# Optimization experiments

Measured on AMD Instinct MI355X. Metric: run time of the kernel, lower is better.

Reference implementation:

```python
import jax, jax.numpy as jnp
import numpy as np

N_HEAD = 16
HEAD_DIM = 64  # n_embd // n_head = 1024 // 16

def setup_inputs() -> dict:
    key = jax.random.key(0)
    k1, k2, k3 = jax.random.split(key, 3)
    B, T, C = 4, 2048, 1024
    x = jax.random.normal(k1, (B, T, C), dtype=jnp.float32)
    w_qkv = jax.random.normal(k2, (3 * C, C), dtype=jnp.float32) * (C ** -0.5)
    w_proj = jax.random.normal(k3, (C, C), dtype=jnp.float32) * (C ** -0.5)
    b_proj = jnp.zeros((C,), dtype=jnp.float32)
    return {"x": x, "w_qkv": w_qkv, "w_proj": w_proj, "b_proj": b_proj}

def reference(x, w_qkv, w_proj, b_proj):
    B, T, C = x.shape
    H, hd = N_HEAD, HEAD_DIM
    # fused QKV projection (no bias), torch Linear: x @ W^T
    qkv = jnp.einsum('btc,dc->btd', x, w_qkv)           # [B,T,3C]
    # module-specific reshape: per-head groups of 3*hd, then chunk into q,k,v
    qkv = qkv.reshape(B, T, H, 3 * hd)
    q, k, v = jnp.split(qkv, 3, axis=-1)                # each [B,T,H,hd]
    q = q.transpose(0, 2, 1, 3)                         # [B,H,T,hd]
    k = k.transpose(0, 2, 1, 3)
    v = v.transpose(0, 2, 1, 3)
    att = jnp.einsum('bhqd,bhkd->bhqk', q, k) * (hd ** -0.5)
    causal = jnp.tril(jnp.ones((T, T), dtype=bool))
    att = jnp.where(causal, att, -jnp.inf)
    att = jax.nn.softmax(att, axis=-1)
    out = jnp.einsum('bhqk,bhkd->bhqd', att, v)         # [B,H,T,hd]
    out = out.transpose(0, 2, 1, 3).reshape(B, T, C)
    out = jnp.einsum('btc,dc->btd', out, w_proj) + b_proj
    return out
```

## Files before the change

kernel.cpp:

```cpp
#include <hip/hip_runtime.h>
#include <hip/hip_bf16.h>

typedef __attribute__((ext_vector_type(8))) short bf16x8;
typedef __attribute__((ext_vector_type(4))) float f32x4;
typedef __attribute__((ext_vector_type(16))) float f32x16;
typedef __attribute__((ext_vector_type(4))) int i32x4;
typedef unsigned short u16;

__device__ __forceinline__ u16 f2bf(float f) {
    __hip_bfloat16 h = __float2bfloat16(f);
    return __builtin_bit_cast(u16, h);
}
__device__ __forceinline__ bf16x8 load8(const u16* p) {
    return *reinterpret_cast<const bf16x8*>(p);
}
__device__ __forceinline__ void gl2lds16(const u16* g, u16* l) {
    __builtin_amdgcn_global_load_lds(
        (const __attribute__((address_space(1))) void*)g,
        (__attribute__((address_space(3))) void*)l, 16, 0, 0);
}
__device__ __forceinline__ unsigned int cvtpk(float lo, float hi) {
    unsigned int r;
    asm("v_cvt_pk_bf16_f32 %0, %1, %2" : "=v"(r) : "v"(lo), "v"(hi));
    return r;
}

#define QSCALE 0.1803368801111244f

__global__ __launch_bounds__(256) void cast_all(
    const float* __restrict__ x, const float* __restrict__ wq,
    const float* __restrict__ wp, u16* __restrict__ Xb,
    u16* __restrict__ Wqb, u16* __restrict__ Wpb)
{
    int i = blockIdx.x * blockDim.x + threadIdx.x;
    const float* s; u16* d; int j;
    if (i < 2097152)      { s = x;  d = Xb;  j = i; }
    else if (i < 2883584) { s = wq; d = Wqb; j = i - 2097152; }
    else                  { s = wp; d = Wpb; j = i - 2883584; }
    float4 f = reinterpret_cast<const float4*>(s)[j];
    ushort4 o;
    o.x = f2bf(f.x); o.y = f2bf(f.y); o.z = f2bf(f.z); o.w = f2bf(f.w);
    reinterpret_cast<ushort4*>(d)[j] = o;
}

#define GEMM256_BODY(EPILOGUE)                                                 \
    const int t = threadIdx.x;                                                 \
    const int lane = t & 63;                                                   \
    const int wave = t >> 6;                                                   \
    const int quad = (lane >> 4);                                              \
    const int lid  = lane & 15;                                                \
    const int wm = wave >> 1;                                                  \
    const int wn = wave & 1;                                                   \
    const int mtile = blockIdx.x * 256;                                        \
    const int ntile = blockIdx.y * 128;                                        \
    const int srow = t >> 2;                                                   \
    const int sk   = (t & 3) * 8;                                              \
    const u16* gA0 = Aptr + (size_t)(mtile + srow) * 1024 + sk;                \
    const u16* gA1 = Aptr + (size_t)(mtile + 128 + srow) * 1024 + sk;          \
    const u16* gA2 = gA0 + 32;                                                 \
    const u16* gA3 = gA1 + 32;                                                 \
    const u16* gB0 = Bptr + (size_t)(ntile + srow) * 1024 + sk;                \
    const u16* gB1 = gB0 + 32;                                                 \
    f32x4 acc[4][4] = {};                                                      \
    STAGE_G(smem, 0)                                                           \
    for (int ks = 0; ks < 16; ++ks) {                                          \
        u16* cb = smem + (ks & 1) * 24576;                                     \
        __syncthreads();                                                       \
        if (ks + 1 < 16) {                                                     \
            u16* nb = smem + ((ks + 1) & 1) * 24576;                           \
            STAGE_G(nb, (ks + 1) * 64)                                         \
        }                                                                      \
        bf16x8 af[4][2], bfr[4][2];                                            \
        _Pragma("unroll")                                                      \
        for (int mi = 0; mi < 4; ++mi)                                         \
            _Pragma("unroll")                                                  \
            for (int kh = 0; kh < 2; ++kh)                                     \
                af[mi][kh] = load8(cb + kh * 8192 +                            \
                    (wm * 64 + mi * 16 + lid) * 32 + quad * 8);                \
        _Pragma("unroll")                                                      \
        for (int ni = 0; ni < 4; ++ni)                                         \
            _Pragma("unroll")                                                  \
            for (int kh = 0; kh < 2; ++kh)                                     \
                bfr[ni][kh] = load8(cb + 16384 + kh * 4096 +                   \
                    (wn * 64 + ni * 16 + lid) * 32 + quad * 8);                \
        __builtin_amdgcn_s_setprio(1);                                         \
        _Pragma("unroll")                                                      \
        for (int mi = 0; mi < 4; ++mi)                                         \
            _Pragma("unroll")                                                  \
            for (int ni = 0; ni < 4; ++ni) {                                   \
                acc[mi][ni] = __builtin_amdgcn_mfma_f32_16x16x32_bf16(         \
                    af[mi][0], bfr[ni][0], acc[mi][ni], 0, 0, 0);              \
                acc[mi][ni] = __builtin_amdgcn_mfma_f32_16x16x32_bf16(         \
                    af[mi][1], bfr[ni][1], acc[mi][ni], 0, 0, 0);              \
            }                                                                  \
        __builtin_amdgcn_s_setprio(0);                                         \
    }                                                                          \
    EPILOGUE

#define STAGE_G(BASE, KK)                                                      \
    {                                                                          \
        gl2lds16(gA0 + (KK), (BASE) + t * 8);                                  \
        gl2lds16(gA1 + (KK), (BASE) + 4096 + t * 8);                           \
        gl2lds16(gA2 + (KK), (BASE) + 8192 + t * 8);                           \
        gl2lds16(gA3 + (KK), (BASE) + 12288 + t * 8);                          \
        gl2lds16(gB0 + (KK), (BASE) + 16384 + t * 8);                          \
        gl2lds16(gB1 + (KK), (BASE) + 20480 + t * 8);                          \
    }

__global__ __launch_bounds__(512, 2) void qkv_gemm256(
    const u16* __restrict__ Aptr, const u16* __restrict__ Bptr,
    u16* __restrict__ Q, u16* __restrict__ K, u16* __restrict__ Vt)
{
    extern __shared__ u16 smem[];
    GEMM256_BODY(
    __syncthreads();
    _Pragma("unroll")
    for (int mi = 0; mi < 4; ++mi)
        _Pragma("unroll")
        for (int ni = 0; ni < 4; ++ni)
            _Pragma("unroll")
            for (int r = 0; r < 4; ++r) {
                int ml = wm * 64 + mi * 16 + quad * 4 + r;
                int m = mtile + ml;
                int n = ntile + wn * 64 + ni * 16 + lid;
                int h = n / 192;
                int rr = n - h * 192;
                int sel = rr >> 6;
                int d = rr & 63;
                float v = acc[mi][ni][r];
                if (sel == 2)
                    smem[d * 258 + ml] = f2bf(v);
                else if (sel == 0)
                    Q[((size_t)h * 8192 + m) * 64 + d] = f2bf(v * QSCALE);
                else
                    K[((size_t)h * 8192 + m) * 64 + d] = f2bf(v);
            }
    __syncthreads();
    for (int d = wave; d < 64; d += 8) {
        int lo = ntile - 128 - d;
        int hh = (lo + 191) / 192;
        int n2 = hh * 192 + 128 + d;
        if (n2 >= ntile && n2 < ntile + 128 && hh < 16) {
            _Pragma("unroll")
            for (int p = 0; p < 2; ++p) {
                int idx = lane + p * 64;
                unsigned int w = (unsigned int)smem[d * 258 + idx * 2]
                               | ((unsigned int)smem[d * 258 + idx * 2 + 1] << 16);
                *reinterpret_cast<unsigned int*>(
                    Vt + ((size_t)(hh * 64 + d)) * 8192 + mtile + idx * 2) = w;
            }
        }
    }
    )
}

__global__ __launch_bounds__(512, 2) void proj_gemm256(
    const u16* __restrict__ Aptr, const u16* __restrict__ Bptr,
    const float* __restrict__ bias, float* __restrict__ out)
{
    extern __shared__ u16 smem[];
    GEMM256_BODY(
    _Pragma("unroll")
    for (int mi = 0; mi < 4; ++mi)
        _Pragma("unroll")
        for (int ni = 0; ni < 4; ++ni)
            _Pragma("unroll")
            for (int r = 0; r < 4; ++r) {
                int m = mtile + wm * 64 + mi * 16 + quad * 4 + r;
                int n = ntile + wn * 64 + ni * 16 + lid;
                out[(size_t)m * 1024 + n] = acc[mi][ni][r] + bias[n];
            }
    )
}

__global__ __launch_bounds__(128, 4) void attn(
    const u16* __restrict__ Q, const u16* __restrict__ K,
    const u16* __restrict__ Vtg, u16* __restrict__ O)
{
    const int qt64 = 31 - (blockIdx.x >> 6);
    const int bh = blockIdx.x & 63;
    const int b = bh >> 4, h = bh & 15;
    const int tid = threadIdx.x;
    const int lane = tid & 63;
    const int wave = tid >> 6;
    const int c31 = lane & 31;
    const int ht  = lane >> 5;

    const size_t hb = ((size_t)h * 8192 + (size_t)b * 2048) * 64;
    const u16* Qp = Q + hb;
    const u16* Kp = K + hb;
    const u16* Vp = Vtg + (size_t)h * 64 * 8192 + (size_t)b * 2048;

    __shared__ __align__(16) u16 Vt[2][64 * 64];

    const int vd = tid >> 3, vslot = tid & 7;
    const int vchunk = vslot ^ (vd & 7);
    const u16* vg = Vp + (size_t)vd * 8192 + vchunk * 8;
    u16* const ldst = (u16*)Vt[0] + vd * 64 + vslot * 8;

#define STAGE(BUFSEL, KK)                                                      \
    {                                                                          \
        u16* d_ = ldst + (BUFSEL) * 4096;                                      \
        _Pragma("unroll")                                                      \
        for (int g = 0; g < 4; ++g)                                            \
            gl2lds16(vg + (size_t)g * 16 * 8192 + (KK), d_ + g * 1024);        \
    }

    const int qw = qt64 * 64 + wave * 32;
    const int q  = qw + c31;

    bf16x8 qf[4];
#pragma unroll
    for (int dm = 0; dm < 4; ++dm)
        qf[dm] = load8(Qp + (size_t)q * 64 + dm * 16 + ht * 8);

    f32x16 od0 = {}, od1 = {};
    float lsum = 0.f;

    const int nkt = qt64 + 1;

    STAGE(0, 0)

#define SOFTMAX_KB(ST, KBOFF, PF0, PF1)                                        \
    {                                                                          \
        float pv[16];                                                          \
        _Pragma("unroll")                                                      \
        for (int r = 0; r < 16; ++r) {                                         \
            const int kg = k0 + (KBOFF) + (r & 3) + 8 * (r >> 2) + 4 * ht;     \
            float sv = ST[r];                                                  \
            if (needmask && kg > q) sv = -1e30f;                               \
            const float p = exp2f(sv);                                         \
            pv[r] = p;                                                         \
            lsum += p;                                                         \
        }                                                                      \
        _Pragma("unroll")                                                      \
        for (int a = 0; a < 2; ++a) {                                          \
            unsigned int u  = cvtpk(pv[8 * a + 0], pv[8 * a + 1]);             \
            unsigned int u2 = cvtpk(pv[8 * a + 2], pv[8 * a + 3]);             \
            unsigned int v  = cvtpk(pv[8 * a + 4], pv[8 * a + 5]);             \
            unsigned int v2 = cvtpk(pv[8 * a + 6], pv[8 * a + 7]);             \
            int r1 = __shfl_xor((int)(ht ? u : v), 32, 64);                    \
            int r2 = __shfl_xor((int)(ht ? u2 : v2), 32, 64);                  \
            i32x4 w;                                                           \
            w.x = ht ? r1 : (int)u;                                            \
            w.y = ht ? r2 : (int)u2;                                           \
            w.z = ht ? (int)v : r1;                                            \
            w.w = ht ? (int)v2 : r2;                                           \
            ((a) ? (PF1) : (PF0)) = __builtin_bit_cast(bf16x8, w);             \
        }                                                                      \
    }

    for (int kt = 0; kt < nkt; ++kt) {
        const int k0 = kt * 64;
        u16* vbuf = Vt[kt & 1];
        const bool skipB = (k0 >= qw);
        const bool needmask = (k0 + 63 > qw);
        bf16x8 pf[4];

        {
            bf16x8 kfA[4];
#pragma unroll
            for (int dm = 0; dm < 4; ++dm)
                kfA[dm] = load8(Kp + (size_t)(k0 + c31) * 64 + dm * 16 + ht * 8);
            f32x16 stA = {};
            __builtin_amdgcn_s_setprio(1);
#pragma unroll
            for (int dm = 0; dm < 4; ++dm)
                stA = __builtin_amdgcn_mfma_f32_32x32x16_bf16(kfA[dm], qf[dm], stA, 0, 0, 0);
            __builtin_amdgcn_s_setprio(0);
            SOFTMAX_KB(stA, 0, pf[0], pf[1]);
        }
        if (!skipB) {
            bf16x8 kfB[4];
#pragma unroll
            for (int dm = 0; dm < 4; ++dm)
                kfB[dm] = load8(Kp + (size_t)(k0 + 32 + c31) * 64 + dm * 16 + ht * 8);
            f32x16 stB = {};
            __builtin_amdgcn_s_setprio(1);
#pragma unroll
            for (int dm = 0; dm < 4; ++dm)
                stB = __builtin_amdgcn_mfma_f32_32x32x16_bf16(kfB[dm], qf[dm], stB, 0, 0, 0);
            __builtin_amdgcn_s_setprio(0);
            SOFTMAX_KB(stB, 32, pf[2], pf[3]);
        }

        __syncthreads();

        if (kt + 1 < nkt) STAGE((kt + 1) & 1, k0 + 64)

        __builtin_amdgcn_s_setprio(1);
#pragma unroll
        for (int km = 0; km < 4; ++km) {
            if (km >= 2 && skipB) continue;
            const int sl = ((km * 2 + ht) ^ (c31 & 7)) * 8;
            bf16x8 v0 = load8(vbuf + c31 * 64 + sl);
            bf16x8 v1 = load8(vbuf + (32 + c31) * 64 + sl);
            od0 = __builtin_amdgcn_mfma_f32_32x32x16_bf16(v0, pf[km], od0, 0, 0, 0);
            od1 = __builtin_amdgcn_mfma_f32_32x32x16_bf16(v1, pf[km], od1, 0, 0, 0);
        }
        __builtin_amdgcn_s_setprio(0);
    }

    const float tot = lsum +
        __builtin_bit_cast(float, __shfl_xor(__builtin_bit_cast(int, lsum), 32, 64));
    const float inv = 1.0f / tot;

    const size_t orow = (size_t)(b * 2048 + q) * 1024 + h * 64;
#pragma unroll
    for (int tp = 0; tp < 8; ++tp) {
        const int r = 2 * tp;
        const int d = (r & 3) + 8 * (r >> 2) + 4 * ht;
        unsigned int w0 = (unsigned int)f2bf(od0[r] * inv) |
                          ((unsigned int)f2bf(od0[r + 1] * inv) << 16);
        unsigned int w1 = (unsigned int)f2bf(od1[r] * inv) |
                          ((unsigned int)f2bf(od1[r + 1] * inv) << 16);
        *reinterpret_cast<unsigned int*>(const_cast<u16*>(O) + orow + d) = w0;
        *reinterpret_cast<unsigned int*>(const_cast<u16*>(O) + orow + 32 + d) = w1;
    }
#undef SOFTMAX_KB
#undef STAGE
}

extern "C" void kernel_launch(void* const* d_in, const int* in_sizes, int n_in,
                              void* d_out, int out_size, void* d_ws, size_t ws_size,
                              hipStream_t stream) {
    const float* x      = (const float*)d_in[0];
    const float* w_qkv  = (const float*)d_in[1];
    const float* w_proj = (const float*)d_in[2];
    const float* b_proj = (const float*)d_in[3];
    float* out = (float*)d_out;

    u16* Q   = (u16*)d_ws;
    u16* K   = Q   + (size_t)16 * 8192 * 64;
    u16* Vt  = K   + (size_t)16 * 8192 * 64;
    u16* A2  = Vt  + (size_t)16 * 64 * 8192;
    u16* Xb  = A2  + (size_t)8192 * 1024;
    u16* Wqb = Xb  + (size_t)8192 * 1024;
    u16* Wpb = Wqb + (size_t)3072 * 1024;

    cast_all<<<dim3(12288), 256, 0, stream>>>(x, w_qkv, w_proj, Xb, Wqb, Wpb);

    qkv_gemm256<<<dim3(32, 24), 512, 98304, stream>>>(Xb, Wqb, Q, K, Vt);
    attn<<<dim3(2048), 128, 0, stream>>>(Q, K, Vt, A2);
    proj_gemm256<<<dim3(32, 8), 512, 98304, stream>>>(A2, Wpb, b_proj, out);
}
```

Measured before the change: 278.3 us.

## Replace 256x128 8-wave GEMM tiles with 128x128 2-wave tiles, K-step 32

Both projection GEMMs move from 512-thread blocks with 256x128 tiles and a 64-wide K step to 128-thread blocks with 128x128 tiles, a 32-wide K step and 128x64 per-wave outputs. The smaller LDS footprint (32 KB) and doubled grid aim to raise occupancy and improve wave scheduling across CUs. In exchange there are twice as many barriers per K loop, LDS traffic per MFMA rises for the A operand, and each wave holds a larger accumulator set, so register pressure increases.

```diff
diff --git a/kernel.cpp b/kernel.cpp
--- a/kernel.cpp
+++ b/kernel.cpp
@@ -43,131 +43,112 @@
     reinterpret_cast<ushort4*>(d)[j] = o;
 }
 
-#define GEMM256_BODY(EPILOGUE)                                                 \
+#define STAGE_W(BASE, KK)                                                      \
+    {                                                                          \
+        _Pragma("unroll")                                                      \
+        for (int g = 0; g < 4; ++g)                                            \
+            gl2lds16(gA + (size_t)g * 32 * 1024 + (KK),                        \
+                     (BASE) + g * 1024 + t * 8);                               \
+        _Pragma("unroll")                                                      \
+        for (int g = 0; g < 4; ++g)                                            \
+            gl2lds16(gB + (size_t)g * 32 * 1024 + (KK),                        \
+                     (BASE) + 4096 + g * 1024 + t * 8);                        \
+    }
+
+#define GEMMW_BODY(EPILOGUE)                                                   \
     const int t = threadIdx.x;                                                 \
     const int lane = t & 63;                                                   \
-    const int wave = t >> 6;                                                   \
-    const int quad = (lane >> 4);                                              \
+    const int wave = t >> 6;                                \
+    const int quad = lane >> 4;                                                \
     const int lid  = lane & 15;                                                \
-    const int wm = wave >> 1;                                                  \
-    const int wn = wave & 1;                                                   \
-    const int mtile = blockIdx.x * 256;                                        \
+    const int mtile = blockIdx.x * 128;                                        \
     const int ntile = blockIdx.y * 128;                                        \
     const int srow = t >> 2;                                                   \
     const int sk   = (t & 3) * 8;                                              \
-    const u16* gA0 = Aptr + (size_t)(mtile + srow) * 1024 + sk;                \
-    const u16* gA1 = Aptr + (size_t)(mtile + 128 + srow) * 1024 + sk;          \
-    const u16* gA2 = gA0 + 32;                                                 \
-    const u16* gA3 = gA1 + 32;                                                 \
-    const u16* gB0 = Bptr + (size_t)(ntile + srow) * 1024 + sk;                \
-    const u16* gB1 = gB0 + 32;                                                 \
-    f32x4 acc[4][4] = {};                                                      \
-    STAGE_G(smem, 0)                                                           \
-    for (int ks = 0; ks < 16; ++ks) {                                          \
-        u16* cb = smem + (ks & 1) * 24576;                                     \
+    const u16* gA = Aptr + (size_t)(mtile + srow) * 1024 + sk;                 \
+    const u16* gB = Bptr + (size_t)(ntile + srow) * 1024 + sk;                 \
+    f32x4 acc[8][4] = {};                                                      \
+    STAGE_W(smem, 0)                                                           \
+    for (int ks = 0; ks < 32; ++ks) {                                          \
+        u16* cb = smem + (ks & 1) * 8192;                                      \
         __syncthreads();                                                       \
-        if (ks + 1 < 16) {                                                     \
-            u16* nb = smem + ((ks + 1) & 1) * 24576;                           \
-            STAGE_G(nb, (ks + 1) * 64)                                         \
-        }                                                                      \
-        bf16x8 af[4][2], bfr[4][2];                                            \
-        _Pragma("unroll")                                                      \
-        for (int mi = 0; mi < 4; ++mi)                                         \
+        if (ks + 1 < 32) STAGE_W(smem + ((ks + 1) & 1) * 8192, (ks + 1) * 32)  \
+        bf16x8 af[8], bfr[4];                                                  \
+        _Pragma("unroll")                                                      \
+        for (int mi = 0; mi < 8; ++mi)                                         \
+            af[mi] = load8(cb + (mi * 16 + lid) * 32 + quad * 8);              \
+        _Pragma("unroll")                                                      \
+        for (int ni = 0; ni < 4; ++ni)                                         \
+            bfr[ni] = load8(cb + 4096 +                                        \
+                (wave * 64 + ni * 16 + lid) * 32 + quad * 8);                  \
+        __builtin_amdgcn_s_setprio(1);                                         \
+        _Pragma("unroll")                                                      \
+        for (int mi = 0; mi < 8; ++mi)                                         \
             _Pragma("unroll")                                                  \
-            for (int kh = 0; kh < 2; ++kh)                                     \
-                af[mi][kh] = load8(cb + kh * 8192 +                            \
-                    (wm * 64 + mi * 16 + lid) * 32 + quad * 8);                \
-        _Pragma("unroll")                                                      \
-        for (int ni = 0; ni < 4; ++ni)                                         \
-            _Pragma("unroll")                                                  \
-            for (int kh = 0; kh < 2; ++kh)                                     \
-                bfr[ni][kh] = load8(cb + 16384 + kh * 4096 +                   \
-                    (wn * 64 + ni * 16 + lid) * 32 + quad * 8);                \
-        __builtin_amdgcn_s_setprio(1);                                         \
-        _Pragma("unroll")                                                      \
-        for (int mi = 0; mi < 4; ++mi)                                         \
-            _Pragma("unroll")                                                  \
-            for (int ni = 0; ni < 4; ++ni) {                                   \
+            for (int ni = 0; ni < 4; ++ni)                                     \
                 acc[mi][ni] = __builtin_amdgcn_mfma_f32_16x16x32_bf16(         \
-                    af[mi][0], bfr[ni][0], acc[mi][ni], 0, 0, 0);              \
-                acc[mi][ni] = __builtin_amdgcn_mfma_f32_16x16x32_bf16(         \
-                    af[mi][1], bfr[ni][1], acc[mi][ni], 0, 0, 0);              \
-            }                                                                  \
+                    af[mi], bfr[ni], acc[mi][ni], 0, 0, 0);                    \
         __builtin_amdgcn_s_setprio(0);                                         \
     }                                                                          \
     EPILOGUE
 
-#define STAGE_G(BASE, KK)                                                      \
-    {                                                                          \
-        gl2lds16(gA0 + (KK), (BASE) + t * 8);                                  \
-        gl2lds16(gA1 + (KK), (BASE) + 4096 + t * 8);                           \
-        gl2lds16(gA2 + (KK), (BASE) + 8192 + t * 8);                           \
-        gl2lds16(gA3 + (KK), (BASE) + 12288 + t * 8);                          \
-        gl2lds16(gB0 + (KK), (BASE) + 16384 + t * 8);                          \
-        gl2lds16(gB1 + (KK), (BASE) + 20480 + t * 8);                          \
-    }
-
-__global__ __launch_bounds__(512, 2) void qkv_gemm256(
+__global__ __launch_bounds__(128, 2) void qkv_gemmw(
     const u16* __restrict__ Aptr, const u16* __restrict__ Bptr,
     u16* __restrict__ Q, u16* __restrict__ K, u16* __restrict__ Vt)
 {
     extern __shared__ u16 smem[];
-    GEMM256_BODY(
+    GEMMW_BODY(
     __syncthreads();
     _Pragma("unroll")
-    for (int mi = 0; mi < 4; ++mi)
+    for (int mi = 0; mi < 8; ++mi)
         _Pragma("unroll")
         for (int ni = 0; ni < 4; ++ni)
             _Pragma("unroll")
             for (int r = 0; r < 4; ++r) {
-                int ml = wm * 64 + mi * 16 + quad * 4 + r;
+                int ml = mi * 16 + quad * 4 + r;
                 int m = mtile + ml;
-                int n = ntile + wn * 64 + ni * 16 + lid;
+                int n = ntile + wave * 64 + ni * 16 + lid;
                 int h = n / 192;
                 int rr = n - h * 192;
                 int sel = rr >> 6;
                 int d = rr & 63;
                 float v = acc[mi][ni][r];
                 if (sel == 2)
-                    smem[d * 258 + ml] = f2bf(v);
+                    smem[d * 130 + ml] = f2bf(v);
                 else if (sel == 0)
                     Q[((size_t)h * 8192 + m) * 64 + d] = f2bf(v * QSCALE);
                 else
                     K[((size_t)h * 8192 + m) * 64 + d] = f2bf(v);
             }
     __syncthreads();
-    for (int d = wave; d < 64; d += 8) {
+    for (int d = wave; d < 64; d += 2) {
         int lo = ntile - 128 - d;
         int hh = (lo + 191) / 192;
         int n2 = hh * 192 + 128 + d;
         if (n2 >= ntile && n2 < ntile + 128 && hh < 16) {
-            _Pragma("unroll")
-            for (int p = 0; p < 2; ++p) {
-                int idx = lane + p * 64;
-                unsigned int w = (unsigned int)smem[d * 258 + idx * 2]
-                               | ((unsigned int)smem[d * 258 + idx * 2 + 1] << 16);
-                *reinterpret_cast<unsigned int*>(
-                    Vt + ((size_t)(hh * 64 + d)) * 8192 + mtile + idx * 2) = w;
-            }
+            unsigned int w = (unsigned int)smem[d * 130 + lane * 2]
+                           | ((unsigned int)smem[d * 130 + lane * 2 + 1] << 16);
+            *reinterpret_cast<unsigned int*>(
+                Vt + ((size_t)(hh * 64 + d)) * 8192 + mtile + lane * 2) = w;
         }
     }
     )
 }
 
-__global__ __launch_bounds__(512, 2) void proj_gemm256(
+__global__ __launch_bounds__(128, 2) void proj_gemmw(
     const u16* __restrict__ Aptr, const u16* __restrict__ Bptr,
     const float* __restrict__ bias, float* __restrict__ out)
 {
     extern __shared__ u16 smem[];
-    GEMM256_BODY(
+    GEMMW_BODY(
     _Pragma("unroll")
-    for (int mi = 0; mi < 4; ++mi)
+    for (int mi = 0; mi < 8; ++mi)
         _Pragma("unroll")
         for (int ni = 0; ni < 4; ++ni)
             _Pragma("unroll")
             for (int r = 0; r < 4; ++r) {
-                int m = mtile + wm * 64 + mi * 16 + quad * 4 + r;
-                int n = ntile + wn * 64 + ni * 16 + lid;
+                int m = mtile + mi * 16 + quad * 4 + r;
+                int n = ntile + wave * 64 + ni * 16 + lid;
                 out[(size_t)m * 1024 + n] = acc[mi][ni][r] + bias[n];
             }
     )
@@ -340,7 +321,7 @@
 
     cast_all<<<dim3(12288), 256, 0, stream>>>(x, w_qkv, w_proj, Xb, Wqb, Wpb);
 
-    qkv_gemm256<<<dim3(32, 24), 512, 98304, stream>>>(Xb, Wqb, Q, K, Vt);
+    qkv_gemmw<<<dim3(64, 24), 128, 32768, stream>>>(Xb, Wqb, Q, K, Vt);
     attn<<<dim3(2048), 128, 0, stream>>>(Q, K, Vt, A2);
-    proj_gemm256<<<dim3(32, 8), 512, 98304, stream>>>(A2, Wpb, b_proj, out);
-}
+    proj_gemmw<<<dim3(64, 8), 128, 32768, stream>>>(A2, Wpb, b_proj, out);
+}
```

After: 291.5 us. 1.05x slower.
